# Optimization experiments

Measured on AMD Instinct MI355X. Metric: run time of the kernel, lower is better.

Reference implementation:

```python
import jax, jax.numpy as jnp
import numpy as np

STRIDE = 4
IMG_H, IMG_W = 800, 1216
NMS_THRESH = 0.7
PRE_NMS = 1000
POST_NMS = 1000
MIN_SIZE = 0.0
SCALE_CLAMP = float(np.log(1000.0 / 16.0))  # detectron2 Box2BoxTransform clamp
A = 3  # anchors per location


def _cell_anchors():
    size = 32.0
    ars = jnp.array([0.5, 1.0, 2.0], jnp.float32)
    area = size * size
    w = jnp.sqrt(area / ars)
    h = ars * w
    return jnp.stack([-w / 2, -h / 2, w / 2, h / 2], axis=1)  # [A,4]


def _anchors(H, W):
    sx = jnp.arange(W, dtype=jnp.float32) * STRIDE
    sy = jnp.arange(H, dtype=jnp.float32) * STRIDE
    gy, gx = jnp.meshgrid(sy, sx, indexing='ij')
    shifts = jnp.stack([gx, gy, gx, gy], axis=-1).reshape(-1, 1, 4)  # [H*W,1,4]
    return (shifts + _cell_anchors()[None]).reshape(-1, 4)  # [H*W*A,4]


def _conv(x, w, b, pad):
    y = jax.lax.conv_general_dilated(x, w, (1, 1), pad,
                                     dimension_numbers=('NCHW', 'OIHW', 'NCHW'))
    return y + b[None, :, None, None]


def _decode(anchors, deltas):
    # anchors [M,4], deltas [N,M,4]; weights (1,1,1,1)
    wa = anchors[:, 2] - anchors[:, 0]
    ha = anchors[:, 3] - anchors[:, 1]
    cx = anchors[:, 0] + 0.5 * wa
    cy = anchors[:, 1] + 0.5 * ha
    dx, dy = deltas[..., 0], deltas[..., 1]
    dw = jnp.minimum(deltas[..., 2], SCALE_CLAMP)
    dh = jnp.minimum(deltas[..., 3], SCALE_CLAMP)
    px = dx * wa + cx
    py = dy * ha + cy
    pw = jnp.exp(dw) * wa
    ph = jnp.exp(dh) * ha
    return jnp.stack([px - 0.5 * pw, py - 0.5 * ph,
                      px + 0.5 * pw, py + 0.5 * ph], axis=-1)


def _iou_matrix(boxes):  # [K,4] -> [K,K]
    area = (boxes[:, 2] - boxes[:, 0]) * (boxes[:, 3] - boxes[:, 1])
    lt = jnp.maximum(boxes[:, None, :2], boxes[None, :, :2])
    rb = jnp.minimum(boxes[:, None, 2:], boxes[None, :, 2:])
    wh = jnp.clip(rb - lt, 0.0)
    inter = wh[..., 0] * wh[..., 1]
    return inter / jnp.maximum(area[:, None] + area[None, :] - inter, 1e-9)


def _nms_keep(boxes):
    # boxes already sorted by descending score; greedy NMS
    iou = _iou_matrix(boxes)
    K = boxes.shape[0]

    def step(sup, i):
        keep = ~sup[i]
        sup = sup | (keep & (iou[i] > NMS_THRESH))
        return sup, keep

    _, keep = jax.lax.scan(step, jnp.zeros(K, bool), jnp.arange(K))
    return keep


def setup_inputs() -> dict:
    key = jax.random.key(0)
    ks = jax.random.split(key, 4)
    features = jax.random.normal(ks[0], (2, 256, 200, 304), jnp.float32)
    w_conv = jax.random.normal(ks[1], (256, 256, 3, 3), jnp.float32) * 0.01
    b_conv = jnp.zeros((256,), jnp.float32)
    w_obj = jax.random.normal(ks[2], (3, 256, 1, 1), jnp.float32) * 0.01
    b_obj = jnp.zeros((3,), jnp.float32)
    w_delta = jax.random.normal(ks[3], (12, 256, 1, 1), jnp.float32) * 0.01
    b_delta = jnp.zeros((12,), jnp.float32)
    return {"features": features, "w_conv": w_conv, "b_conv": b_conv,
            "w_obj": w_obj, "b_obj": b_obj, "w_delta": w_delta, "b_delta": b_delta}


def reference(features, w_conv, b_conv, w_obj, b_obj, w_delta, b_delta):
    N, C, H, W = features.shape
    t = jax.nn.relu(_conv(features, w_conv, b_conv, 'SAME'))
    logits = _conv(t, w_obj, b_obj, 'VALID')            # [N,A,H,W]
    deltas = _conv(t, w_delta, b_delta, 'VALID')        # [N,4A,H,W]
    logits = logits.transpose(0, 2, 3, 1).reshape(N, -1)               # [N,H*W*A]
    deltas = deltas.reshape(N, A, 4, H, W).transpose(0, 3, 4, 1, 2).reshape(N, -1, 4)

    anchors = _anchors(H, W)                             # [H*W*A,4]
    boxes = _decode(anchors, deltas)                     # [N,M,4]
    boxes = jnp.stack([jnp.clip(boxes[..., 0], 0.0, IMG_W),
                       jnp.clip(boxes[..., 1], 0.0, IMG_H),
                       jnp.clip(boxes[..., 2], 0.0, IMG_W),
                       jnp.clip(boxes[..., 3], 0.0, IMG_H)], axis=-1)

    valid = ((boxes[..., 2] - boxes[..., 0]) >= MIN_SIZE) & \
            ((boxes[..., 3] - boxes[..., 1]) >= MIN_SIZE)
    scores = jnp.where(valid, logits, -jnp.inf)

    top_s, top_i = jax.lax.top_k(scores, PRE_NMS)                      # sorted desc
    top_b = jnp.take_along_axis(boxes, top_i[..., None], axis=1)       # [N,K,4]

    keep = jax.vmap(_nms_keep)(top_b)                                  # [N,K]
    s = jnp.where(keep, top_s, -jnp.inf)
    fin_s, fin_i = jax.lax.top_k(s, POST_NMS)                          # sorted desc (=final sort)
    fin_b = jnp.take_along_axis(top_b, fin_i[..., None], axis=1)
    fin_b = jnp.where(jnp.isfinite(fin_s)[..., None], fin_b, 0.0)
    return fin_b, fin_s
```

## Files before the change

### kernel.cpp

```cpp
#include <hip/hip_runtime.h>
#include <math.h>
#include <stdint.h>

#define CC 256
#define HH 200
#define WW 304
#define NN 2
#define HW 60800
#define MM 182400
#define KK 1000
#define HP 202
#define WP 306
#define SCALE_CLAMP_F 4.135166556742356f
#define NEG_SENTINEL -1.0e30f
#define CAND_CAP 2048

typedef __attribute__((ext_vector_type(8))) short short8;
typedef __attribute__((ext_vector_type(4))) float f32x4;

#define VMW(N) asm volatile("s_waitcnt vmcnt(" #N ")" ::: "memory")

__device__ __forceinline__ unsigned short f2bf(float f) {
  unsigned u = __float_as_uint(f);
  u += 0x7FFFu + ((u >> 16) & 1u);
  return (unsigned short)(u >> 16);
}
__device__ __forceinline__ unsigned int fkey(float s) {
  unsigned int u = __float_as_uint(s);
  return (u & 0x80000000u) ? ~u : (u | 0x80000000u);
}
__device__ __forceinline__ float iou_ref(float4 a, float4 b) {
#pragma clang fp contract(off)
  float areaA = (a.z - a.x) * (a.w - a.y);
  float areaB = (b.z - b.x) * (b.w - b.y);
  float ltx = fmaxf(a.x, b.x), lty = fmaxf(a.y, b.y);
  float rbx = fminf(a.z, b.z), rby = fminf(a.w, b.w);
  float w = fmaxf(rbx - ltx, 0.0f), h = fmaxf(rby - lty, 0.0f);
  float inter = w * h;
  float denom = fmaxf(areaA + areaB - inter, 1e-9f);
  return inter / denom;
}
__device__ __forceinline__ void gload16(const void* g, void* l) {
  __builtin_amdgcn_global_load_lds(
      (const __attribute__((address_space(1))) unsigned int*)g,
      (__attribute__((address_space(3))) unsigned int*)l, 16, 0, 0);
}
__device__ __forceinline__ int swz(int byte) {
  return byte ^ (((byte >> 7) & 7) << 4);
}

__global__ __launch_bounds__(256) void wt_pack(const float* __restrict__ w,
                                               unsigned short* __restrict__ wt_b) {
  int o = blockIdx.x * 256 + threadIdx.x;
  int cin = o & 255, cout = (o >> 8) & 255, pos = o >> 16;
  wt_b[o] = f2bf(w[(cout * 256 + cin) * 9 + pos]);
}

__global__ __launch_bounds__(256) void in_pack(const float* __restrict__ in,
                                               unsigned short* __restrict__ fbp) {
  __shared__ unsigned short tile[64][65];
  int tid = threadIdx.x;
  int p0 = blockIdx.x * 64;
  int c0 = blockIdx.y * 64;
  int n = blockIdx.z;
  int lane = tid & 63;
  int p = p0 + lane;
  int yp = 0, xp = 0;
  bool inb = false;
  if (p < HP * WP) {
    yp = p / WP; xp = p - yp * WP;
    inb = (yp >= 1 && yp <= HH && xp >= 1 && xp <= WW);
  }
  for (int ci = tid >> 6; ci < 64; ci += 4) {
    float v = 0.f;
    if (inb) v = in[(((size_t)n * CC + c0 + ci) * HH + (yp - 1)) * WW + (xp - 1)];
    tile[ci][lane] = f2bf(v);
  }
  __syncthreads();
  for (int i = 0; i < 4; ++i) {
    int idx4 = (i * 256 + tid) * 4;
    int hwi = idx4 >> 6, cb = idx4 & 63;
    int pp = p0 + hwi;
    if (pp < HP * WP) {
      ushort4 v;
      v.x = tile[cb][hwi]; v.y = tile[cb + 1][hwi];
      v.z = tile[cb + 2][hwi]; v.w = tile[cb + 3][hwi];
      *(ushort4*)&fbp[((size_t)n * HP * WP + pp) * 256 + c0 + cb] = v;
    }
  }
}

__global__ __launch_bounds__(256) void conv_mfma(
    const unsigned short* __restrict__ wt_b, const unsigned short* __restrict__ fbp,
    const float* __restrict__ bias, const float* __restrict__ w_obj,
    const float* __restrict__ w_delta, float* __restrict__ phead) {
  __shared__ __align__(16) unsigned short lA[3][4096];
  __shared__ __align__(16) unsigned short lB[2][5760];
  __shared__ float bl_l[128];
  int tid = threadIdx.x;
  int lane = tid & 63, wid = tid >> 6;
  int wm = wid >> 1, wn = wid & 1;
  int lrow = lane & 15, lgrp = lane >> 4;
  int zz = blockIdx.z;
  int n = zz >> 1, ct = zz & 1;
  int X0 = blockIdx.x * 16, Y0 = blockIdx.y * 8;

  f32x4 acc[4][4];
#pragma unroll
  for (int m = 0; m < 4; ++m)
#pragma unroll
    for (int r = 0; r < 4; ++r) acc[m][r] = {0.f, 0.f, 0.f, 0.f};

  if (tid < 128) bl_l[tid] = bias[ct * 128 + tid];

  auto stageA = [&](int pos, int cc, int buf) {
#pragma unroll
    for (int is = 0; is < 2; ++is) {
      int idx = is * 256 + tid;
      int L = swz(idx * 16);
      int cout = L >> 6, q = (L >> 4) & 3;
      const unsigned short* g =
          wt_b + (((size_t)pos * 256 + ct * 128 + cout) << 8) + cc * 32 + q * 8;
      gload16(g, (char*)&lA[buf][0] + is * 4096 + (wid << 10));
    }
  };
  auto stageB = [&](int cc, int buf) {
#pragma unroll
    for (int is = 0; is < 3; ++is) {
      int idx = is * 256 + tid;
      if (idx < 720) {
        int L = swz(idx * 16);
        int rc = L >> 6, q = (L >> 4) & 3;
        int row = rc / 18, col = rc - row * 18;
        const unsigned short* g =
            fbp + (((size_t)n * HP + Y0 + row) * WP + X0 + col) * 256 + cc * 32 + q * 8;
        gload16(g, (char*)&lB[buf][0] + is * 4096 + (wid << 10));
      }
    }
  };

  stageA(0, 0, 0);
  stageA(1, 0, 1);
  stageB(0, 0);
  __syncthreads();

#pragma unroll 1
  for (int cc = 0; cc < 8; ++cc) {
    const int bb = cc & 1;
    const bool ccl7 = (cc < 7);
#pragma unroll
    for (int pos = 0; pos < 9; ++pos) {
      {
        int pos2 = pos + 2, cc2 = cc;
        if (pos2 >= 9) { pos2 -= 9; cc2 += 1; }
        if (cc2 < 8) stageA(pos2, cc2, (pos + 2) % 3);
      }
      if (pos == 0 && ccl7) stageB(cc + 1, bb ^ 1);

      int ky = pos / 3, kx = pos - ky * 3;
      short8 af[4], bfr[4];
#pragma unroll
      for (int m = 0; m < 4; ++m) {
        int Lb = ((wm * 64 + m * 16 + lrow) << 6) + (lgrp << 4);
        af[m] = *(const short8*)((const char*)&lA[pos % 3][0] + swz(Lb));
      }
#pragma unroll
      for (int r = 0; r < 4; ++r) {
        int Lb = (((wn * 4 + r + ky) * 18 + lrow + kx) << 6) + (lgrp << 4);
        bfr[r] = *(const short8*)((const char*)&lB[bb][0] + swz(Lb));
      }
#pragma unroll
      for (int m = 0; m < 4; ++m)
#pragma unroll
        for (int r = 0; r < 4; ++r)
          acc[m][r] = __builtin_amdgcn_mfma_f32_16x16x32_bf16(af[m], bfr[r], acc[m][r], 0, 0, 0);

      if (pos < 2) {
        if (ccl7) VMW(5); else VMW(2);
      } else if (pos == 7) {
        if (ccl7) VMW(2); else VMW(0);
      } else {
        VMW(2);
      }
      __builtin_amdgcn_sched_barrier(0);
      __builtin_amdgcn_s_barrier();
      asm volatile("" ::: "memory");
    }
  }
  __syncthreads();

#pragma unroll
  for (int m = 0; m < 4; ++m)
#pragma unroll
    for (int j = 0; j < 4; ++j) {
      float b = bl_l[wm * 64 + m * 16 + (lgrp << 2) + j];
#pragma unroll
      for (int r = 0; r < 4; ++r) acc[m][r][j] = fmaxf(acc[m][r][j] + b, 0.f);
    }

  float* whl_l = (float*)&lA[0][0];
  for (int i = tid; i < 1920; i += 256) {
    int o = i >> 7, cl = i & 127;
    whl_l[i] = (o < 3) ? w_obj[o * 256 + ct * 128 + cl]
                       : w_delta[(o - 3) * 256 + ct * 128 + cl];
  }
  __syncthreads();

  float* hacc = (float*)&lB[0][0];
#pragma unroll 1
  for (int o = 0; o < 15; ++o) {
    float p0 = 0.f, p1 = 0.f, p2 = 0.f, p3 = 0.f;
#pragma unroll
    for (int m = 0; m < 4; ++m)
#pragma unroll
      for (int j = 0; j < 4; ++j) {
        float w = whl_l[o * 128 + wm * 64 + m * 16 + (lgrp << 2) + j];
        p0 = fmaf(w, acc[m][0][j], p0);
        p1 = fmaf(w, acc[m][1][j], p1);
        p2 = fmaf(w, acc[m][2][j], p2);
        p3 = fmaf(w, acc[m][3][j], p3);
      }
    p0 += __shfl_xor(p0, 16); p0 += __shfl_xor(p0, 32);
    p1 += __shfl_xor(p1, 16); p1 += __shfl_xor(p1, 32);
    p2 += __shfl_xor(p2, 16); p2 += __shfl_xor(p2, 32);
    p3 += __shfl_xor(p3, 16); p3 += __shfl_xor(p3, 32);
    if (lgrp == 0) {
      hacc[(((o * 8) + wn * 4 + 0) * 16 + lrow) * 2 + wm] = p0;
      hacc[(((o * 8) + wn * 4 + 1) * 16 + lrow) * 2 + wm] = p1;
      hacc[(((o * 8) + wn * 4 + 2) * 16 + lrow) * 2 + wm] = p2;
      hacc[(((o * 8) + wn * 4 + 3) * 16 + lrow) * 2 + wm] = p3;
    }
  }
  __syncthreads();

  if (tid < 128) {
    int row = tid >> 4, col = tid & 15;
    int loc = (Y0 + row) * WW + (X0 + col);
    size_t base = ((size_t)zz * 15) * HW + loc;
#pragma unroll
    for (int o = 0; o < 15; ++o) {
      const float* hp = &hacc[((o * 8 + row) * 16 + col) * 2];
      phead[base + (size_t)o * HW] = hp[0] + hp[1];
    }
  }
}

__global__ __launch_bounds__(256) void decode_kernel(
    const float* __restrict__ phead, const float* __restrict__ b_obj,
    const float* __restrict__ b_delta, float* __restrict__ scores,
    float* __restrict__ boxes, unsigned long long* __restrict__ keys,
    unsigned int* __restrict__ ghist) {
  __shared__ unsigned int hl[8192];
  int tid = threadIdx.x;
  for (int i = tid; i < 8192; i += 256) hl[i] = 0;
  __syncthreads();
  int n = blockIdx.y;
  int loc = blockIdx.x * 256 + tid;
  if (loc < HW) {
    float ho[15];
    const float* p0 = phead + ((size_t)(n * 2 + 0) * 15) * HW + loc;
    const float* p1 = phead + ((size_t)(n * 2 + 1) * 15) * HW + loc;
#pragma unroll
    for (int o = 0; o < 15; ++o) ho[o] = p0[(size_t)o * HW] + p1[(size_t)o * HW];
#pragma unroll
    for (int o = 0; o < 3; ++o) ho[o] += b_obj[o];
#pragma unroll
    for (int o = 0; o < 12; ++o) ho[3 + o] += b_delta[o];
    {
#pragma clang fp contract(off)
      int h = loc / WW, w = loc - h * WW;
      float gx = (float)(w * 4);
      float gy = (float)(h * 4);
      float s2048 = sqrtf(2048.0f), s512 = sqrtf(512.0f);
      float aw[3] = {s2048, 32.0f, s512};
      float ah[3] = {0.5f * s2048, 32.0f, 2.0f * s512};
#pragma unroll
      for (int a = 0; a < 3; ++a) {
        float ax1 = gx - 0.5f * aw[a], ay1 = gy - 0.5f * ah[a];
        float ax2 = gx + 0.5f * aw[a], ay2 = gy + 0.5f * ah[a];
        float wa = ax2 - ax1, ha = ay2 - ay1;
        float cx = ax1 + 0.5f * wa, cy = ay1 + 0.5f * ha;
        float dx = ho[3 + a * 4 + 0], dy = ho[3 + a * 4 + 1];
        float dw = fminf(ho[3 + a * 4 + 2], SCALE_CLAMP_F);
        float dh = fminf(ho[3 + a * 4 + 3], SCALE_CLAMP_F);
        float px = dx * wa + cx, py = dy * ha + cy;
        float pw = expf(dw) * wa, ph = expf(dh) * ha;
        float x1 = px - 0.5f * pw, y1 = py - 0.5f * ph;
        float x2v = px + 0.5f * pw, y2v = py + 0.5f * ph;
        x1 = fminf(fmaxf(x1, 0.f), 1216.f);
        y1 = fminf(fmaxf(y1, 0.f), 800.f);
        x2v = fminf(fmaxf(x2v, 0.f), 1216.f);
        y2v = fminf(fmaxf(y2v, 0.f), 800.f);
        int m = loc * 3 + a;
        ((float4*)boxes)[(size_t)n * MM + m] = make_float4(x1, y1, x2v, y2v);
        float sc = ho[a];
        scores[(size_t)n * MM + m] = sc;
        unsigned long long k =
            ((unsigned long long)fkey(sc) << 18) | (unsigned long long)(262143 - m);
        keys[(size_t)n * MM + m] = k;
        atomicAdd(&hl[(unsigned)(k >> 37)], 1u);
      }
    }
  }
  __syncthreads();
  for (int i = tid; i < 8192; i += 256) {
    unsigned v = hl[i];
    if (v) atomicAdd(&ghist[n * 8192 + i], v);
  }
}

__global__ __launch_bounds__(256) void gather_kernel(
    const unsigned long long* __restrict__ keys, const unsigned int* __restrict__ ghist,
    unsigned int* __restrict__ cnt, unsigned long long* __restrict__ cand) {
  __shared__ unsigned int ps[256];
  __shared__ int bsh;
  int n = blockIdx.y, tid = threadIdx.x;
  const unsigned int* h = ghist + n * 8192;
  unsigned s = 0;
  for (int k = 0; k < 32; ++k) s += h[tid * 32 + k];
  ps[tid] = s;
  __syncthreads();
  if (tid == 0) {
    unsigned cum = 0; int b = 0;
    for (int t = 255; t >= 0; --t) {
      if (cum + ps[t] >= KK) {
        for (int bin = t * 32 + 31; bin >= t * 32; --bin) {
          cum += h[bin];
          if (cum >= KK) { b = bin; break; }
        }
        break;
      }
      cum += ps[t];
    }
    bsh = b;
  }
  __syncthreads();
  int b = bsh;
  const unsigned long long* kp = keys + (size_t)n * MM;
  int i0 = blockIdx.x * 2850, i1 = min(i0 + 2850, MM);
  for (int i = i0 + tid; i < i1; i += 256) {
    unsigned long long k = kp[i];
    if ((int)(unsigned)(k >> 37) >= b) {
      unsigned pos = atomicAdd(&cnt[n], 1u);
      if (pos < CAND_CAP) cand[(size_t)n * CAND_CAP + pos] = k;
    }
  }
}

__global__ __launch_bounds__(1024) void final_select(
    const unsigned long long* __restrict__ cand, const unsigned int* __restrict__ cnt,
    const float* __restrict__ scores, const float* __restrict__ boxes,
    float* __restrict__ s_scores, float* __restrict__ s_boxes) {
  __shared__ unsigned long long sel[CAND_CAP];
  int n = blockIdx.x, tid = threadIdx.x;
  int E = (int)min(cnt[n], (unsigned)CAND_CAP);
  for (int i = tid; i < CAND_CAP; i += 1024)
    sel[i] = (i < E) ? cand[(size_t)n * CAND_CAP + i] : 0ull;
  __syncthreads();
  for (unsigned k2 = 2; k2 <= CAND_CAP; k2 <<= 1) {
    for (unsigned j = k2 >> 1; j > 0; j >>= 1) {
      for (int i = tid; i < CAND_CAP; i += 1024) {
        int l = i ^ (int)j;
        if (l > i) {
          unsigned long long a = sel[i], bb = sel[l];
          bool sw = ((i & k2) == 0) ? (a < bb) : (a > bb);
          if (sw) { sel[i] = bb; sel[l] = a; }
        }
      }
      __syncthreads();
    }
  }
  if (tid < KK) {
    unsigned long long k = sel[tid];
    int m = 262143 - (int)(k & 0x3FFFFull);
    s_scores[n * KK + tid] = scores[(size_t)n * MM + m];
    ((float4*)s_boxes)[n * KK + tid] = ((const float4*)boxes)[(size_t)n * MM + m];
  }
}

__global__ __launch_bounds__(256) void mask_kernel(const float* __restrict__ s_boxes,
                                                   unsigned long long* __restrict__ mask) {
  int i = blockIdx.x, n = blockIdx.y;
  int tid = threadIdx.x, w = tid >> 6, lane = tid & 63;
  const float4* bp = (const float4*)s_boxes + n * KK;
  float4 bi = bp[i];
#pragma unroll
  for (int p = 0; p < 4; ++p) {
    int word = p * 4 + w;
    int j = word * 64 + lane;
    bool over = false;
    if (j < KK) {
      float4 bj = bp[j];
      over = iou_ref(bi, bj) > 0.7f;
    }
    unsigned long long bal = __ballot(over);
    if (lane == 0) mask[((size_t)n * KK + i) * 16 + word] = bal;
  }
}

__global__ __launch_bounds__(1024) void scan_write_kernel(
    const float* __restrict__ s_scores, const float* __restrict__ s_boxes,
    const unsigned long long* __restrict__ mask, float* __restrict__ out) {
  int n = blockIdx.x, tid = threadIdx.x;
  int wid = tid >> 6, lane = tid & 63;
  __shared__ unsigned long long swl[16];
  __shared__ unsigned long long keepw[16];
  __shared__ unsigned int wpre[17];
  if (tid < 16) swl[tid] = 0ull;
  __syncthreads();
  const unsigned long long* mrow = mask + (size_t)n * 16000;
  for (int c = 0; c < 16; ++c) {
    int i = c * 64 + lane;
    unsigned long long myword = (i < KK) ? mrow[(size_t)i * 16 + wid] : 0ull;
    if (wid == 0) {
      unsigned long long m = (i < KK) ? mrow[(size_t)i * 16 + c] : 0ull;
      unsigned long long cur = swl[c];
      unsigned long long kw = 0ull;
      int lim = min(64, KK - c * 64);
      for (int b = 0; b < lim; ++b) {
        unsigned long long mb = __shfl(m, b);
        if (!((cur >> b) & 1ull)) { kw |= (1ull << b); cur |= mb; }
      }
      if (lane == 0) keepw[c] = kw;
    }
    __syncthreads();
    unsigned long long kw = keepw[c];
    unsigned long long v = ((kw >> lane) & 1ull) ? myword : 0ull;
#pragma unroll
    for (int s = 32; s > 0; s >>= 1) v |= __shfl_xor(v, s);
    if (lane == 0) swl[wid] |= v;
    __syncthreads();
  }
  if (tid == 0) {
    unsigned int c = 0;
    for (int w2 = 0; w2 < 16; ++w2) { wpre[w2] = c; c += (unsigned int)__popcll(keepw[w2]); }
    wpre[16] = c;
  }
  __syncthreads();
  if (tid < KK) {
    int word = tid >> 6, bit = tid & 63;
    unsigned long long kwv = keepw[word];
    bool kept = (kwv >> bit) & 1ull;
    unsigned int before = wpre[word] + (unsigned int)__popcll(kwv & ((1ull << bit) - 1ull));
    unsigned int nk = wpre[16];
    unsigned int dst = kept ? before : nk + ((unsigned int)tid - before);
    float4 b = kept ? ((const float4*)s_boxes)[n * KK + tid] : make_float4(0.f, 0.f, 0.f, 0.f);
    float s = kept ? s_scores[n * KK + tid] : NEG_SENTINEL;
    ((float4*)out)[n * KK + dst] = b;
    out[8000 + n * KK + dst] = s;
  }
}

extern "C" void kernel_launch(void* const* d_in, const int* in_sizes, int n_in,
                              void* d_out, int out_size, void* d_ws, size_t ws_size,
                              hipStream_t stream) {
  (void)in_sizes; (void)n_in; (void)out_size; (void)ws_size;
  const float* features = (const float*)d_in[0];
  const float* w_conv   = (const float*)d_in[1];
  const float* b_conv   = (const float*)d_in[2];
  const float* w_obj    = (const float*)d_in[3];
  const float* b_obj    = (const float*)d_in[4];
  const float* w_delta  = (const float*)d_in[5];
  const float* b_delta  = (const float*)d_in[6];

  char* ws = (char*)d_ws;
  unsigned short* wt_b = (unsigned short*)ws;
  unsigned short* fbp  = (unsigned short*)(ws + 1179648);
  char* O = ws + 64475136;
  float* phead = (float*)O;
  float* scores = (float*)(O + 14592000);
  float* boxes  = (float*)(O + 16051200);
  unsigned long long* keys = (unsigned long long*)(O + 21888000);
  char* P = O + 24806400;
  unsigned int* ghist = (unsigned int*)P;
  unsigned int* cnt = (unsigned int*)(P + 65536);
  unsigned long long* cand = (unsigned long long*)(P + 65792);
  float* s_scores = (float*)(P + 98560);
  float* s_boxes  = (float*)(P + 106752);
  unsigned long long* maskbuf = (unsigned long long*)(P + 139264);
  float* out = (float*)d_out;

  wt_pack<<<2304, 256, 0, stream>>>(w_conv, wt_b);
  in_pack<<<dim3(966, 4, 2), 256, 0, stream>>>(features, fbp);
  hipMemsetAsync(ghist, 0, 65536 + 256, stream);
  conv_mfma<<<dim3(19, 25, 4), 256, 0, stream>>>(wt_b, fbp, b_conv, w_obj, w_delta, phead);
  decode_kernel<<<dim3(238, 2), 256, 0, stream>>>(phead, b_obj, b_delta,
                                                  scores, boxes, keys, ghist);
  gather_kernel<<<dim3(64, 2), 256, 0, stream>>>(keys, ghist, cnt, cand);
  final_select<<<2, 1024, 0, stream>>>(cand, cnt, scores, boxes, s_scores, s_boxes);
  mask_kernel<<<dim3(1000, 2), 256, 0, stream>>>(s_boxes, maskbuf);
  scan_write_kernel<<<2, 1024, 0, stream>>>(s_scores, s_boxes, maskbuf, out);
}
```

Before: 395.6 us.

## Merge pack kernels and memset into one launch; double-buffer conv weight staging

The weight pack, input pack and histogram/counter zeroing are merged into a single kernel with block-range dispatch, replacing two launches and a memset. In the conv MFMA main loop, the weight tile staging drops from a triple buffer with a prefetch distance of two to a double buffer with a prefetch distance of one. The hand-tuned partial vmcnt waits plus raw s_barrier are replaced by plain __syncthreads. This saves LDS and launch overhead, but it shortens how far loads run ahead and likely forces full memory waits every step, which can expose load latency in the dominant conv kernel.

```diff
diff --git a/kernel.cpp b/kernel.cpp
--- a/kernel.cpp
+++ b/kernel.cpp
@@ -18,8 +18,6 @@
 typedef __attribute__((ext_vector_type(8))) short short8;
 typedef __attribute__((ext_vector_type(4))) float f32x4;
 
-#define VMW(N) asm volatile("s_waitcnt vmcnt(" #N ")" ::: "memory")
-
 __device__ __forceinline__ unsigned short f2bf(float f) {
   unsigned u = __float_as_uint(f);
   u += 0x7FFFu + ((u >> 16) & 1u);
@@ -49,44 +47,51 @@
   return byte ^ (((byte >> 7) & 7) << 4);
 }
 
-__global__ __launch_bounds__(256) void wt_pack(const float* __restrict__ w,
-                                               unsigned short* __restrict__ wt_b) {
-  int o = blockIdx.x * 256 + threadIdx.x;
-  int cin = o & 255, cout = (o >> 8) & 255, pos = o >> 16;
-  wt_b[o] = f2bf(w[(cout * 256 + cin) * 9 + pos]);
-}
-
-__global__ __launch_bounds__(256) void in_pack(const float* __restrict__ in,
-                                               unsigned short* __restrict__ fbp) {
+__global__ __launch_bounds__(256) void pack_kernel(
+    const float* __restrict__ w, unsigned short* __restrict__ wt_b,
+    const float* __restrict__ in, unsigned short* __restrict__ fbp,
+    unsigned int* __restrict__ ghist, unsigned int* __restrict__ cnt) {
   __shared__ unsigned short tile[64][65];
+  int b = blockIdx.x;
   int tid = threadIdx.x;
-  int p0 = blockIdx.x * 64;
-  int c0 = blockIdx.y * 64;
-  int n = blockIdx.z;
-  int lane = tid & 63;
-  int p = p0 + lane;
-  int yp = 0, xp = 0;
-  bool inb = false;
-  if (p < HP * WP) {
-    yp = p / WP; xp = p - yp * WP;
-    inb = (yp >= 1 && yp <= HH && xp >= 1 && xp <= WW);
-  }
-  for (int ci = tid >> 6; ci < 64; ci += 4) {
-    float v = 0.f;
-    if (inb) v = in[(((size_t)n * CC + c0 + ci) * HH + (yp - 1)) * WW + (xp - 1)];
-    tile[ci][lane] = f2bf(v);
-  }
-  __syncthreads();
-  for (int i = 0; i < 4; ++i) {
-    int idx4 = (i * 256 + tid) * 4;
-    int hwi = idx4 >> 6, cb = idx4 & 63;
-    int pp = p0 + hwi;
-    if (pp < HP * WP) {
-      ushort4 v;
-      v.x = tile[cb][hwi]; v.y = tile[cb + 1][hwi];
-      v.z = tile[cb + 2][hwi]; v.w = tile[cb + 3][hwi];
-      *(ushort4*)&fbp[((size_t)n * HP * WP + pp) * 256 + c0 + cb] = v;
-    }
+  if (b < 2304) {
+    int o = b * 256 + tid;
+    int cin = o & 255, cout = (o >> 8) & 255, pos = o >> 16;
+    wt_b[o] = f2bf(w[(cout * 256 + cin) * 9 + pos]);
+  } else if (b < 10032) {
+    int bb = b - 2304;
+    int bx = bb % 966, rem = bb / 966;
+    int by = rem & 3, n = rem >> 2;
+    int p0 = bx * 64, c0 = by * 64;
+    int lane = tid & 63;
+    int p = p0 + lane;
+    int yp = 0, xp = 0;
+    bool inb = false;
+    if (p < HP * WP) {
+      yp = p / WP; xp = p - yp * WP;
+      inb = (yp >= 1 && yp <= HH && xp >= 1 && xp <= WW);
+    }
+    for (int ci = tid >> 6; ci < 64; ci += 4) {
+      float v = 0.f;
+      if (inb) v = in[(((size_t)n * CC + c0 + ci) * HH + (yp - 1)) * WW + (xp - 1)];
+      tile[ci][lane] = f2bf(v);
+    }
+    __syncthreads();
+    for (int i = 0; i < 4; ++i) {
+      int idx4 = (i * 256 + tid) * 4;
+      int hwi = idx4 >> 6, cb = idx4 & 63;
+      int pp = p0 + hwi;
+      if (pp < HP * WP) {
+        ushort4 v;
+        v.x = tile[cb][hwi]; v.y = tile[cb + 1][hwi];
+        v.z = tile[cb + 2][hwi]; v.w = tile[cb + 3][hwi];
+        *(ushort4*)&fbp[((size_t)n * HP * WP + pp) * 256 + c0 + cb] = v;
+      }
+    }
+  } else {
+    int i = (b - 10032) * 256 + tid;
+    ghist[i] = 0;
+    if (i < 2) cnt[i] = 0;
   }
 }
 
@@ -94,7 +99,7 @@
     const unsigned short* __restrict__ wt_b, const unsigned short* __restrict__ fbp,
     const float* __restrict__ bias, const float* __restrict__ w_obj,
     const float* __restrict__ w_delta, float* __restrict__ phead) {
-  __shared__ __align__(16) unsigned short lA[3][4096];
+  __shared__ __align__(16) unsigned short lA[2][4096];
   __shared__ __align__(16) unsigned short lB[2][5760];
   __shared__ float bl_l[128];
   int tid = threadIdx.x;
@@ -140,29 +145,24 @@
   };
 
   stageA(0, 0, 0);
-  stageA(1, 0, 1);
   stageB(0, 0);
   __syncthreads();
 
+  int ab = 0;
 #pragma unroll 1
   for (int cc = 0; cc < 8; ++cc) {
-    const int bb = cc & 1;
-    const bool ccl7 = (cc < 7);
+    int bb = cc & 1;
 #pragma unroll
     for (int pos = 0; pos < 9; ++pos) {
-      {
-        int pos2 = pos + 2, cc2 = cc;
-        if (pos2 >= 9) { pos2 -= 9; cc2 += 1; }
-        if (cc2 < 8) stageA(pos2, cc2, (pos + 2) % 3);
-      }
-      if (pos == 0 && ccl7) stageB(cc + 1, bb ^ 1);
-
+      if (pos < 8) stageA(pos + 1, cc, ab ^ 1);
+      else if (cc < 7) stageA(0, cc + 1, ab ^ 1);
+      if (pos == 0 && cc < 7) stageB(cc + 1, bb ^ 1);
       int ky = pos / 3, kx = pos - ky * 3;
       short8 af[4], bfr[4];
 #pragma unroll
       for (int m = 0; m < 4; ++m) {
         int Lb = ((wm * 64 + m * 16 + lrow) << 6) + (lgrp << 4);
-        af[m] = *(const short8*)((const char*)&lA[pos % 3][0] + swz(Lb));
+        af[m] = *(const short8*)((const char*)&lA[ab][0] + swz(Lb));
       }
 #pragma unroll
       for (int r = 0; r < 4; ++r) {
@@ -174,20 +174,10 @@
 #pragma unroll
         for (int r = 0; r < 4; ++r)
           acc[m][r] = __builtin_amdgcn_mfma_f32_16x16x32_bf16(af[m], bfr[r], acc[m][r], 0, 0, 0);
-
-      if (pos < 2) {
-        if (ccl7) VMW(5); else VMW(2);
-      } else if (pos == 7) {
-        if (ccl7) VMW(2); else VMW(0);
-      } else {
-        VMW(2);
-      }
-      __builtin_amdgcn_sched_barrier(0);
-      __builtin_amdgcn_s_barrier();
-      asm volatile("" ::: "memory");
-    }
-  }
-  __syncthreads();
+      __syncthreads();
+      ab ^= 1;
+    }
+  }
 
 #pragma unroll
   for (int m = 0; m < 4; ++m)
@@ -480,9 +470,7 @@
   unsigned long long* maskbuf = (unsigned long long*)(P + 139264);
   float* out = (float*)d_out;
 
-  wt_pack<<<2304, 256, 0, stream>>>(w_conv, wt_b);
-  in_pack<<<dim3(966, 4, 2), 256, 0, stream>>>(features, fbp);
-  hipMemsetAsync(ghist, 0, 65536 + 256, stream);
+  pack_kernel<<<10096, 256, 0, stream>>>(w_conv, wt_b, features, fbp, ghist, cnt);
   conv_mfma<<<dim3(19, 25, 4), 256, 0, stream>>>(wt_b, fbp, b_conv, w_obj, w_delta, phead);
   decode_kernel<<<dim3(238, 2), 256, 0, stream>>>(phead, b_obj, b_delta,
                                                   scores, boxes, keys, ghist);
```

Measured after the change: 388.5 us. No clear change (-1.8%).
